# Performance work log

Measured on AMD Instinct MI355X. Metric: run time of the kernel, lower is better.

The kernel has to match this reference:

```python
import jax, jax.numpy as jnp
import numpy as np

E, K, H, I = 16, 4, 2048, 1024
B, S = 1, 2048


def setup_inputs() -> dict:
    key = jax.random.key(0)
    ks = jax.random.split(key, 5)
    scale_in = 1.0 / np.sqrt(H)
    scale_mid = 1.0 / np.sqrt(I)
    return {
        "x": jax.random.normal(ks[0], (B, S, H), dtype=jnp.float32),
        "gate_w": jax.random.normal(ks[1], (E, H), dtype=jnp.float32) * scale_in,
        "w1_gate": jax.random.normal(ks[2], (E, I, H), dtype=jnp.float32) * scale_in,
        "w1_up": jax.random.normal(ks[3], (E, I, H), dtype=jnp.float32) * scale_in,
        "w2": jax.random.normal(ks[4], (E, H, I), dtype=jnp.float32) * scale_mid,
        "topk": K,
    }


def reference(x, gate_w, w1_gate, w1_up, w2, topk):
    orig_shape = x.shape
    xt = x.reshape(-1, x.shape[-1])            # [T, H]
    T = xt.shape[0]
    n_exp = gate_w.shape[0]

    # Router: top-k logits, softmax over the selected k (as in the torch code).
    logits = xt @ gate_w.T                      # [T, E]
    topk_vals, topk_ids = jax.lax.top_k(logits, topk)
    topk_w = jax.nn.softmax(topk_vals, axis=-1)  # [T, K]

    # Dense per-token-per-expert combine weight; 0 for unselected experts.
    # Mathematically identical to the gather/scatter-add loop: unselected
    # experts contribute expert_out * 0.
    gate_dense = jnp.zeros((T, n_exp), dtype=xt.dtype)
    gate_dense = gate_dense.at[jnp.arange(T)[:, None], topk_ids].add(topk_w)

    # SwiGLU per expert (dense over experts; weights zero-out unused ones).
    g = jnp.einsum("th,eih->tei", xt, w1_gate)   # [T, E, I]
    u = jnp.einsum("th,eih->tei", xt, w1_up)     # [T, E, I]
    h = jax.nn.silu(g) * u                        # [T, E, I]
    out = jnp.einsum("tei,te,ehi->th", h, gate_dense, w2)  # [T, H]
    return out.reshape(orig_shape)
```

## Files before the change

kernel.cpp:

```cpp
#include <hip/hip_runtime.h>
#include <hip/hip_bf16.h>
#include <stdint.h>

#define NEXP 16
#define KSEL 4
#define HDIM 2048
#define IDIM 1024
#define TTOK 2048
#define NT1 16
#define NTB 16
#define MAXT1 47
#define MAXB1 (MAXT1 * NT1)
#define MAXBB (MAXT1 * NTB)
#define NCVT 1024
#define NCVT1 512
#define NW8 ((NEXP * IDIM * HDIM) / 8)

typedef __attribute__((ext_vector_type(8))) short bf16x8;
typedef __attribute__((ext_vector_type(4))) float f32x4;
typedef unsigned int u32;

__device__ __forceinline__ uint32_t pack2(float a, float b) {
  __hip_bfloat162 h = __float22bfloat162_rn(float2{a, b});
  uint32_t u;
  __builtin_memcpy(&u, &h, 4);
  return u;
}
__device__ __forceinline__ ushort bf1(float a) {
  __hip_bfloat16 h = __float2bfloat16(a);
  ushort u;
  __builtin_memcpy(&u, &h, 2);
  return u;
}
__device__ __forceinline__ void gload16(const void* g, void* l) {
  __builtin_amdgcn_global_load_lds(
      (const __attribute__((address_space(1))) u32*)g,
      (__attribute__((address_space(3))) u32*)l, 16, 0, 0);
}
__device__ __forceinline__ int swzread(int row, int q) {
  return row * 32 + ((q ^ ((row >> 1) & 3)) << 3);
}
__device__ __forceinline__ void cvt_bodyN(const float* __restrict__ src,
                                          ushort* __restrict__ dst,
                                          int idx0, int stride) {
  for (int i = idx0; i < NW8; i += stride) {
    f32x4 a = __builtin_nontemporal_load(((const f32x4*)src) + i * 2);
    f32x4 b = __builtin_nontemporal_load(((const f32x4*)src) + i * 2 + 1);
    uint4 t;
    t.x = pack2(a[0], a[1]); t.y = pack2(a[2], a[3]);
    t.z = pack2(b[0], b[1]); t.w = pack2(b[2], b[3]);
    ((uint4*)dst)[i] = t;
  }
}

__global__ __launch_bounds__(256) void router_kernel(
    const float* __restrict__ x, const float* __restrict__ gw,
    ushort* __restrict__ xb, int* __restrict__ topk_id,
    float* __restrict__ topk_w,
    const float* __restrict__ srcG, ushort* __restrict__ dstG,
    const float* __restrict__ srcU, ushort* __restrict__ dstU)
{
  if (blockIdx.x >= TTOK / 4 + NCVT) {
    cvt_bodyN(srcU, dstU,
              (blockIdx.x - (TTOK / 4 + NCVT)) * 256 + threadIdx.x, NCVT * 256);
    return;
  }
  if (blockIdx.x >= TTOK / 4) {
    cvt_bodyN(srcG, dstG,
              (blockIdx.x - TTOK / 4) * 256 + threadIdx.x, NCVT * 256);
    return;
  }
  const int wid = threadIdx.x >> 6;
  const int lane = threadIdx.x & 63;
  const int t = blockIdx.x * 4 + wid;
  const float4* x4 = (const float4*)(x + (size_t)t * HDIM);
  const float4* gw4 = (const float4*)gw;
  float acc[NEXP];
#pragma unroll
  for (int e = 0; e < NEXP; ++e) acc[e] = 0.f;
#pragma unroll
  for (int i = 0; i < HDIM / 256; ++i) {
    const int idx = i * 64 + lane;
    float4 xv = x4[idx];
    uint2 xp;
    xp.x = pack2(xv.x, xv.y);
    xp.y = pack2(xv.z, xv.w);
    *(uint2*)(xb + (size_t)t * HDIM + idx * 4) = xp;
#pragma unroll
    for (int e = 0; e < NEXP; ++e) {
      float4 wv = gw4[e * (HDIM / 4) + idx];
      acc[e] += xv.x * wv.x + xv.y * wv.y + xv.z * wv.z + xv.w * wv.w;
    }
  }
#pragma unroll
  for (int e = 0; e < NEXP; ++e) {
#pragma unroll
    for (int off = 32; off >= 1; off >>= 1)
      acc[e] += __shfl_xor(acc[e], off);
  }
  if (lane == 0) {
    unsigned taken = 0;
    float vals[KSEL];
    int ids[KSEL];
#pragma unroll
    for (int k = 0; k < KSEL; ++k) {
      float bv = -3.4e38f; int bi = 0;
      for (int e = 0; e < NEXP; ++e)
        if (!((taken >> e) & 1u) && acc[e] > bv) { bv = acc[e]; bi = e; }
      taken |= 1u << bi; vals[k] = bv; ids[k] = bi;
    }
    float m = vals[0], s = 0.f, w[KSEL];
#pragma unroll
    for (int k = 0; k < KSEL; ++k) { w[k] = __expf(vals[k] - m); s += w[k]; }
    float is = 1.f / s;
#pragma unroll
    for (int k = 0; k < KSEL; ++k) {
      topk_id[t * KSEL + k] = ids[k];
      topk_w[t * KSEL + k] = w[k] * is;
    }
  }
}

__global__ __launch_bounds__(1024) void plan_scatter_kernel(
    const int* __restrict__ topk_id, int* __restrict__ counts,
    int* __restrict__ offsets, int* __restrict__ nWA, int* __restrict__ nWB,
    int* __restrict__ wlA, int* __restrict__ wlB,
    int* __restrict__ rowTok, int* __restrict__ inv)
{
  __shared__ int cnt[NEXP], off[NEXP], cur[NEXP];
  __shared__ int t1[NEXP], p1[NEXP];
  const int tid = threadIdx.x;
  if (tid < NEXP) { cnt[tid] = 0; cur[tid] = 0; }
  __syncthreads();
  for (int i = tid; i < TTOK * KSEL; i += 1024)
    atomicAdd(&cnt[topk_id[i]], 1);
  __syncthreads();
  if (tid == 0) {
    int s = 0, a = 0;
    for (int e = 0; e < NEXP; ++e) {
      off[e] = s; s += cnt[e];
      t1[e] = (cnt[e] + 255) >> 8;  p1[e] = a;  a += t1[e];
    }
    *nWA = a * NT1;
    *nWB = a * NTB;
  }
  __syncthreads();
  if (tid < NEXP) {
    counts[tid] = cnt[tid];
    offsets[tid] = off[tid];
    const int e = tid, T = t1[e];
    int idx = p1[e] * NT1;
    for (int nt = 0; nt < NT1; ++nt)
      for (int mt = 0; mt < T; ++mt)
        wlA[idx++] = (e << 12) | (nt << 6) | mt;
  } else if (tid < 2 * NEXP) {
    const int e = tid - NEXP, T = t1[e];
    int idx = p1[e] * NTB;
    for (int nt = 0; nt < NTB; ++nt)
      for (int mt = 0; mt < T; ++mt)
        wlB[idx++] = (e << 12) | (nt << 6) | mt;
  }
  for (int i = tid; i < TTOK * KSEL; i += 1024) {
    const int e = topk_id[i];
    const int pos = atomicAdd(&cur[e], 1);
    const int row = off[e] + pos;
    rowTok[row] = i >> 2;
    inv[i] = row;
  }
}

__global__ __launch_bounds__(512) void gemm1_kernel(
    const ushort* __restrict__ xb,
    const ushort* __restrict__ wG, const ushort* __restrict__ wU,
    const int* __restrict__ rowTok, const int* __restrict__ counts,
    const int* __restrict__ offsets, const int* __restrict__ nW,
    const int* __restrict__ wl, ushort* __restrict__ hbuf,
    const float* __restrict__ cvsrc, ushort* __restrict__ cvdst)
{
  if (blockIdx.x >= MAXB1) {
    cvt_bodyN(cvsrc, cvdst,
              (blockIdx.x - MAXB1) * 512 + threadIdx.x, NCVT1 * 512);
    return;
  }
  const int nTot = *nW;
  const int L = (blockIdx.x & 7) * (MAXB1 / 8) + (blockIdx.x >> 3);
  if (L >= nTot) return;
  const int w = wl[L];
  const int e = w >> 12, nt = (w >> 6) & 63, mt = w & 63;
  const int n_e = counts[e], rowbase = offsets[e];

  __shared__ ushort As[2][256 * 32];
  __shared__ ushort Bg[2][64 * 32];
  __shared__ ushort Bu[2][64 * 32];

  const int tid = threadIdx.x;
  const int lane = tid & 63;
  const int wid = tid >> 6;

  const int lr4 = lane >> 2;
  const int ckA = lane & 3;
  const int arl0 = wid * 32 + lr4;
  const int arl1 = wid * 32 + 16 + lr4;
  const int schA0 = (ckA ^ ((arl0 >> 1) & 3)) << 3;
  const int schA1 = (ckA ^ ((arl1 >> 1) & 3)) << 3;
  const int ag0 = mt * 256 + arl0, ag1 = mt * 256 + arl1;
  const int tok0 = rowTok[rowbase + (ag0 < n_e ? ag0 : n_e - 1)];
  const int tok1 = rowTok[rowbase + (ag1 < n_e ? ag1 : n_e - 1)];
  const ushort* pA0 = xb + (size_t)tok0 * HDIM + schA0;
  const ushort* pA1 = xb + (size_t)tok1 * HDIM + schA1;
  const int brl = (wid & 3) * 16 + lr4;
  const int schB = (ckA ^ ((brl >> 1) & 3)) << 3;
  const size_t wbase = (size_t)e * IDIM * HDIM;
  const ushort* pB = ((wid < 4) ? wG : wU) + wbase +
                     (size_t)(nt * 64 + brl) * HDIM + schB;

  const int wr = (wid >> 1) << 6;
  const int wc = (wid & 1) << 5;
  const int lr = lane & 15;
  const int q = lane >> 4;

  f32x4 accG[4][2], accU[4][2];
#pragma unroll
  for (int i = 0; i < 4; ++i)
#pragma unroll
    for (int j = 0; j < 2; ++j) {
      accG[i][j] = (f32x4){0.f, 0.f, 0.f, 0.f};
      accU[i][j] = (f32x4){0.f, 0.f, 0.f, 0.f};
    }

  auto STAGE = [&](int b) {
    gload16(pA0, &As[b][wid * 1024 + lane * 8]);
    gload16(pA1, &As[b][wid * 1024 + 512 + lane * 8]);
    if (wid < 4) gload16(pB, &Bg[b][wid * 512 + lane * 8]);
    else         gload16(pB, &Bu[b][(wid - 4) * 512 + lane * 8]);
    pA0 += 32; pA1 += 32; pB += 32;
  };

  const int NTK = HDIM / 32;
  STAGE(0);
  __syncthreads();
  int buf = 0;
  for (int kt = 0; kt < NTK; ++kt) {
    if (kt + 1 < NTK) STAGE(buf ^ 1);
    bf16x8 af[4], bg[2], bu[2];
#pragma unroll
    for (int mi = 0; mi < 4; ++mi)
      af[mi] = *(const bf16x8*)&As[buf][swzread(wr + mi * 16 + lr, q)];
#pragma unroll
    for (int ni = 0; ni < 2; ++ni) {
      bg[ni] = *(const bf16x8*)&Bg[buf][swzread(wc + ni * 16 + lr, q)];
      bu[ni] = *(const bf16x8*)&Bu[buf][swzread(wc + ni * 16 + lr, q)];
    }
#pragma unroll
    for (int mi = 0; mi < 4; ++mi)
#pragma unroll
      for (int ni = 0; ni < 2; ++ni) {
        accG[mi][ni] = __builtin_amdgcn_mfma_f32_16x16x32_bf16(af[mi], bg[ni], accG[mi][ni], 0, 0, 0);
        accU[mi][ni] = __builtin_amdgcn_mfma_f32_16x16x32_bf16(af[mi], bu[ni], accU[mi][ni], 0, 0, 0);
      }
    __syncthreads();
    buf ^= 1;
  }

#pragma unroll
  for (int mi = 0; mi < 4; ++mi) {
#pragma unroll
    for (int ni = 0; ni < 2; ++ni) {
      const int col = nt * 64 + wc + ni * 16 + lr;
#pragma unroll
      for (int r = 0; r < 4; ++r) {
        const int mrow = mt * 256 + wr + mi * 16 + q * 4 + r;
        if (mrow < n_e) {
          const float gv = accG[mi][ni][r];
          const float uv = accU[mi][ni][r];
          const float hv = (gv / (1.f + __expf(-gv))) * uv;
          hbuf[(size_t)(rowbase + mrow) * IDIM + col] = bf1(hv);
        }
      }
    }
  }
}

__global__ __launch_bounds__(512) void gemmB_kernel(
    const ushort* __restrict__ hb, const ushort* __restrict__ wb,
    const int* __restrict__ counts, const int* __restrict__ offsets,
    const int* __restrict__ nW, const int* __restrict__ wl,
    ushort* __restrict__ po)
{
  const int nTot = *nW;
  const int L = (blockIdx.x & 7) * (MAXBB / 8) + (blockIdx.x >> 3);
  if (L >= nTot) return;
  const int w = wl[L];
  const int e = w >> 12, nt = (w >> 6) & 63, mt = w & 63;
  const int n_e = counts[e], rowbase = offsets[e];

  __shared__ ushort As[2][256 * 32];
  __shared__ ushort Bs[2][128 * 32];

  const int tid = threadIdx.x;
  const int lane = tid & 63;
  const int wid = tid >> 6;

  const int lr4 = lane >> 2;
  const int ckA = lane & 3;
  const int arl0 = wid * 32 + lr4;
  const int arl1 = wid * 32 + 16 + lr4;
  const int schA0 = (ckA ^ ((arl0 >> 1) & 3)) << 3;
  const int schA1 = (ckA ^ ((arl1 >> 1) & 3)) << 3;
  const int ag0 = mt * 256 + arl0, ag1 = mt * 256 + arl1;
  const int g0 = rowbase + (ag0 < n_e ? ag0 : n_e - 1);
  const int g1 = rowbase + (ag1 < n_e ? ag1 : n_e - 1);
  const ushort* pA0 = hb + (size_t)g0 * IDIM + schA0;
  const ushort* pA1 = hb + (size_t)g1 * IDIM + schA1;
  const int brl = wid * 16 + lr4;
  const int schB = (ckA ^ ((brl >> 1) & 3)) << 3;
  const size_t wbase = (size_t)e * HDIM * IDIM;
  const ushort* pB = wb + wbase + (size_t)(nt * 128 + brl) * IDIM + schB;

  const int wr = (wid >> 1) << 6;
  const int wc = (wid & 1) << 6;
  const int lr = lane & 15;
  const int q = lane >> 4;

  f32x4 acc[4][4];
#pragma unroll
  for (int i = 0; i < 4; ++i)
#pragma unroll
    for (int j = 0; j < 4; ++j) acc[i][j] = (f32x4){0.f, 0.f, 0.f, 0.f};

  auto STAGE = [&](int b) {
    gload16(pA0, &As[b][wid * 1024 + lane * 8]);
    gload16(pA1, &As[b][wid * 1024 + 512 + lane * 8]);
    gload16(pB, &Bs[b][wid * 512 + lane * 8]);
    pA0 += 32; pA1 += 32; pB += 32;
  };

  const int NTK = IDIM / 32;
  STAGE(0);
  __syncthreads();
  int buf = 0;
  for (int kt = 0; kt < NTK; ++kt) {
    if (kt + 1 < NTK) STAGE(buf ^ 1);
    bf16x8 af[4], bfr[4];
#pragma unroll
    for (int mi = 0; mi < 4; ++mi)
      af[mi] = *(const bf16x8*)&As[buf][swzread(wr + mi * 16 + lr, q)];
#pragma unroll
    for (int ni = 0; ni < 4; ++ni)
      bfr[ni] = *(const bf16x8*)&Bs[buf][swzread(wc + ni * 16 + lr, q)];
#pragma unroll
    for (int mi = 0; mi < 4; ++mi)
#pragma unroll
      for (int ni = 0; ni < 4; ++ni)
        acc[mi][ni] = __builtin_amdgcn_mfma_f32_16x16x32_bf16(af[mi], bfr[ni], acc[mi][ni], 0, 0, 0);
    __syncthreads();
    buf ^= 1;
  }

#pragma unroll
  for (int mi = 0; mi < 4; ++mi) {
#pragma unroll
    for (int ni = 0; ni < 4; ++ni) {
      const int col = nt * 128 + wc + ni * 16 + lr;
#pragma unroll
      for (int r = 0; r < 4; ++r) {
        const int mrow = mt * 256 + wr + mi * 16 + q * 4 + r;
        if (mrow < n_e)
          po[(size_t)(rowbase + mrow) * HDIM + col] = bf1(acc[mi][ni][r]);
      }
    }
  }
}

__global__ __launch_bounds__(256) void combine_kernel(
    const ushort* __restrict__ po, const int* __restrict__ inv,
    const float* __restrict__ tw, float* __restrict__ out)
{
  const int t = blockIdx.x;
  const int r0 = inv[t * 4 + 0], r1 = inv[t * 4 + 1];
  const int r2 = inv[t * 4 + 2], r3 = inv[t * 4 + 3];
  const float w0 = tw[t * 4 + 0], w1 = tw[t * 4 + 1];
  const float w2v = tw[t * 4 + 2], w3 = tw[t * 4 + 3];
  const int i = threadIdx.x;
  uint4 v0 = *(const uint4*)(po + (size_t)r0 * HDIM + i * 8);
  uint4 v1 = *(const uint4*)(po + (size_t)r1 * HDIM + i * 8);
  uint4 v2 = *(const uint4*)(po + (size_t)r2 * HDIM + i * 8);
  uint4 v3 = *(const uint4*)(po + (size_t)r3 * HDIM + i * 8);
  float o[8];
#pragma unroll
  for (int w = 0; w < 4; ++w) {
    const uint32_t a = (&v0.x)[w], b = (&v1.x)[w], c = (&v2.x)[w], d = (&v3.x)[w];
    o[w * 2 + 0] = w0 * __builtin_bit_cast(float, a << 16) +
                   w1 * __builtin_bit_cast(float, b << 16) +
                   w2v * __builtin_bit_cast(float, c << 16) +
                   w3 * __builtin_bit_cast(float, d << 16);
    o[w * 2 + 1] = w0 * __builtin_bit_cast(float, a & 0xffff0000u) +
                   w1 * __builtin_bit_cast(float, b & 0xffff0000u) +
                   w2v * __builtin_bit_cast(float, c & 0xffff0000u) +
                   w3 * __builtin_bit_cast(float, d & 0xffff0000u);
  }
  float4* o4 = (float4*)(out + (size_t)t * HDIM + i * 8);
  o4[0] = (float4){o[0], o[1], o[2], o[3]};
  o4[1] = (float4){o[4], o[5], o[6], o[7]};
}

extern "C" void kernel_launch(void* const* d_in, const int* in_sizes, int n_in,
                              void* d_out, int out_size, void* d_ws, size_t ws_size,
                              hipStream_t stream) {
  const float* x   = (const float*)d_in[0];
  const float* gw  = (const float*)d_in[1];
  const float* w1g = (const float*)d_in[2];
  const float* w1u = (const float*)d_in[3];
  const float* w2  = (const float*)d_in[4];
  float* out = (float*)d_out;

  char* ws = (char*)d_ws;
  ushort* xb    = (ushort*)(ws + 0);
  ushort* wbufG = (ushort*)(ws + 8388608);
  ushort* wbufU = (ushort*)(ws + 75497472);
  ushort* wbuf2 = (ushort*)(ws + 142606336);
  ushort* hbuf  = (ushort*)(ws + 209715200);
  ushort* po    = (ushort*)(ws + 226492416);
  int*    tkid   = (int*)(ws + 260046848);
  float*  tkw    = (float*)(ws + 260046848 + 32768);
  int*    rowTok = (int*)(ws + 260046848 + 65536);
  int*    inv    = (int*)(ws + 260046848 + 98304);
  int*    ctrl   = (int*)(ws + 260177920);
  int* counts  = ctrl;
  int* offsets = ctrl + 32;
  int* nWA     = ctrl + 50;
  int* nWB     = ctrl + 51;
  int* wlA     = ctrl + 64;
  int* wlB     = ctrl + 64 + MAXB1;

  router_kernel<<<TTOK / 4 + 2 * NCVT, 256, 0, stream>>>(
      x, gw, xb, tkid, tkw, w1g, wbufG, w1u, wbufU);
  plan_scatter_kernel<<<1, 1024, 0, stream>>>(tkid, counts, offsets, nWA, nWB,
                                              wlA, wlB, rowTok, inv);
  gemm1_kernel<<<MAXB1 + NCVT1, 512, 0, stream>>>(
      xb, wbufG, wbufU, rowTok, counts, offsets, nWA, wlA, hbuf,
      w2, wbuf2);
  gemmB_kernel<<<MAXBB, 512, 0, stream>>>(hbuf, wbuf2, counts, offsets,
                                          nWB, wlB, po);
  combine_kernel<<<TTOK, 256, 0, stream>>>(po, inv, tkw, out);
}
```

Baseline: 310.2 us.

## Restructure gemm1 into 128-row tiles with triple-buffered loads and split gate/up waves

The first MoE GEMM drops from 256-row to 128-row M tiles, which roughly doubles its grid and gives it a separate worklist size from the second GEMM. Its shared-memory pipeline goes from double to triple buffering, with explicit vmcnt waits and raw barriers so two stages of loads stay in flight. Each wave now computes either the gate or the up product instead of both, and the up results are passed through LDS to the gate waves for the SwiGLU epilogue. This aims at more parallelism and better latency hiding, at the cost of an extra LDS exchange plus barrier and lower arithmetic reuse per tile.

After: 309.4 us. Within noise of the previous version (-0.2%).

```diff
diff --git a/kernel.cpp b/kernel.cpp
--- a/kernel.cpp
+++ b/kernel.cpp
@@ -9,9 +9,10 @@
 #define TTOK 2048
 #define NT1 16
 #define NTB 16
-#define MAXT1 47
+#define MAXT1 80
 #define MAXB1 (MAXT1 * NT1)
-#define MAXBB (MAXT1 * NTB)
+#define MAXTB 47
+#define MAXBB (MAXTB * NTB)
 #define NCVT 1024
 #define NCVT1 512
 #define NW8 ((NEXP * IDIM * HDIM) / 8)
@@ -128,7 +129,7 @@
     int* __restrict__ rowTok, int* __restrict__ inv)
 {
   __shared__ int cnt[NEXP], off[NEXP], cur[NEXP];
-  __shared__ int t1[NEXP], p1[NEXP];
+  __shared__ int t1[NEXP], p1[NEXP], tB[NEXP], pB[NEXP];
   const int tid = threadIdx.x;
   if (tid < NEXP) { cnt[tid] = 0; cur[tid] = 0; }
   __syncthreads();
@@ -136,13 +137,14 @@
     atomicAdd(&cnt[topk_id[i]], 1);
   __syncthreads();
   if (tid == 0) {
-    int s = 0, a = 0;
+    int s = 0, a = 0, b = 0;
     for (int e = 0; e < NEXP; ++e) {
       off[e] = s; s += cnt[e];
-      t1[e] = (cnt[e] + 255) >> 8;  p1[e] = a;  a += t1[e];
+      t1[e] = (cnt[e] + 127) >> 7;  p1[e] = a;  a += t1[e];
+      tB[e] = (cnt[e] + 255) >> 8;  pB[e] = b;  b += tB[e];
     }
     *nWA = a * NT1;
-    *nWB = a * NTB;
+    *nWB = b * NTB;
   }
   __syncthreads();
   if (tid < NEXP) {
@@ -154,8 +156,8 @@
       for (int mt = 0; mt < T; ++mt)
         wlA[idx++] = (e << 12) | (nt << 6) | mt;
   } else if (tid < 2 * NEXP) {
-    const int e = tid - NEXP, T = t1[e];
-    int idx = p1[e] * NTB;
+    const int e = tid - NEXP, T = tB[e];
+    int idx = pB[e] * NTB;
     for (int nt = 0; nt < NTB; ++nt)
       for (int mt = 0; mt < T; ++mt)
         wlB[idx++] = (e << 12) | (nt << 6) | mt;
@@ -189,96 +191,119 @@
   const int e = w >> 12, nt = (w >> 6) & 63, mt = w & 63;
   const int n_e = counts[e], rowbase = offsets[e];
 
-  __shared__ ushort As[2][256 * 32];
-  __shared__ ushort Bg[2][64 * 32];
-  __shared__ ushort Bu[2][64 * 32];
+  __shared__ ushort lds[24576];
+#define AS(b) (lds + (b) * 4096)
+#define BG(b) (lds + 12288 + (b) * 2048)
+#define BU(b) (lds + 18432 + (b) * 2048)
 
   const int tid = threadIdx.x;
   const int lane = tid & 63;
-  const int wid = tid >> 6;
-
-  const int lr4 = lane >> 2;
-  const int ckA = lane & 3;
-  const int arl0 = wid * 32 + lr4;
-  const int arl1 = wid * 32 + 16 + lr4;
-  const int schA0 = (ckA ^ ((arl0 >> 1) & 3)) << 3;
-  const int schA1 = (ckA ^ ((arl1 >> 1) & 3)) << 3;
-  const int ag0 = mt * 256 + arl0, ag1 = mt * 256 + arl1;
-  const int tok0 = rowTok[rowbase + (ag0 < n_e ? ag0 : n_e - 1)];
-  const int tok1 = rowTok[rowbase + (ag1 < n_e ? ag1 : n_e - 1)];
-  const ushort* pA0 = xb + (size_t)tok0 * HDIM + schA0;
-  const ushort* pA1 = xb + (size_t)tok1 * HDIM + schA1;
-  const int brl = (wid & 3) * 16 + lr4;
-  const int schB = (ckA ^ ((brl >> 1) & 3)) << 3;
+  const int wv = tid >> 6;
+
+  const int arow = tid >> 2;
+  const int ckA = tid & 3;
+  const int schA = (ckA ^ ((arow >> 1) & 3)) << 3;
+  const int agr = mt * 128 + arow;
+  const int tokA = rowTok[rowbase + (agr < n_e ? agr : n_e - 1)];
+  const ushort* pA = xb + (size_t)tokA * HDIM + schA;
+  const int bloc = tid & 255;
+  const int brow = bloc >> 2;
+  const int ckB = bloc & 3;
+  const int schB = (ckB ^ ((brow >> 1) & 3)) << 3;
   const size_t wbase = (size_t)e * IDIM * HDIM;
-  const ushort* pB = ((wid < 4) ? wG : wU) + wbase +
-                     (size_t)(nt * 64 + brl) * HDIM + schB;
-
-  const int wr = (wid >> 1) << 6;
-  const int wc = (wid & 1) << 5;
+  const ushort* pB = ((tid < 256) ? wG : wU) + wbase +
+                     (size_t)(nt * 64 + brow) * HDIM + schB;
+
+  const int wr = (wv >> 2) << 6;
+  const int ng = wv & 3;
+  const bool isU = ng >= 2;
+  const int wc = (ng & 1) << 5;
   const int lr = lane & 15;
   const int q = lane >> 4;
 
-  f32x4 accG[4][2], accU[4][2];
+  f32x4 acc[4][2];
 #pragma unroll
   for (int i = 0; i < 4; ++i)
 #pragma unroll
-    for (int j = 0; j < 2; ++j) {
-      accG[i][j] = (f32x4){0.f, 0.f, 0.f, 0.f};
-      accU[i][j] = (f32x4){0.f, 0.f, 0.f, 0.f};
-    }
+    for (int j = 0; j < 2; ++j) acc[i][j] = (f32x4){0.f, 0.f, 0.f, 0.f};
 
   auto STAGE = [&](int b) {
-    gload16(pA0, &As[b][wid * 1024 + lane * 8]);
-    gload16(pA1, &As[b][wid * 1024 + 512 + lane * 8]);
-    if (wid < 4) gload16(pB, &Bg[b][wid * 512 + lane * 8]);
-    else         gload16(pB, &Bu[b][(wid - 4) * 512 + lane * 8]);
-    pA0 += 32; pA1 += 32; pB += 32;
+    gload16(pA, AS(b) + tid * 8);
+    if (tid < 256) gload16(pB, BG(b) + bloc * 8);
+    else           gload16(pB, BU(b) + bloc * 8);
+    pA += 32; pB += 32;
   };
 
   const int NTK = HDIM / 32;
   STAGE(0);
-  __syncthreads();
+  STAGE(1);
+  asm volatile("s_waitcnt vmcnt(2)" ::: "memory");
+  __builtin_amdgcn_s_barrier();
+  __builtin_amdgcn_sched_barrier(0);
   int buf = 0;
   for (int kt = 0; kt < NTK; ++kt) {
-    if (kt + 1 < NTK) STAGE(buf ^ 1);
-    bf16x8 af[4], bg[2], bu[2];
-#pragma unroll
-    for (int mi = 0; mi < 4; ++mi)
-      af[mi] = *(const bf16x8*)&As[buf][swzread(wr + mi * 16 + lr, q)];
-#pragma unroll
-    for (int ni = 0; ni < 2; ++ni) {
-      bg[ni] = *(const bf16x8*)&Bg[buf][swzread(wc + ni * 16 + lr, q)];
-      bu[ni] = *(const bf16x8*)&Bu[buf][swzread(wc + ni * 16 + lr, q)];
-    }
+    if (kt + 2 < NTK) STAGE(buf == 0 ? 2 : buf - 1);
+    const ushort* bsrc = isU ? BU(buf) : BG(buf);
+    bf16x8 af[4], bf[2];
+#pragma unroll
+    for (int mi = 0; mi < 4; ++mi)
+      af[mi] = *(const bf16x8*)&AS(buf)[swzread(wr + mi * 16 + lr, q)];
+#pragma unroll
+    for (int ni = 0; ni < 2; ++ni)
+      bf[ni] = *(const bf16x8*)&bsrc[swzread(wc + ni * 16 + lr, q)];
+#pragma unroll
+    for (int mi = 0; mi < 4; ++mi)
+#pragma unroll
+      for (int ni = 0; ni < 2; ++ni)
+        acc[mi][ni] = __builtin_amdgcn_mfma_f32_16x16x32_bf16(af[mi], bf[ni], acc[mi][ni], 0, 0, 0);
+    if (kt + 1 < NTK) {
+      if (kt + 2 < NTK)
+        asm volatile("s_waitcnt vmcnt(2)" ::: "memory");
+      else
+        asm volatile("s_waitcnt vmcnt(0)" ::: "memory");
+      __builtin_amdgcn_s_barrier();
+      __builtin_amdgcn_sched_barrier(0);
+    }
+    buf = (buf == 2) ? 0 : buf + 1;
+  }
+
+  __syncthreads();
+  float* uex = (float*)lds;
+  if (isU) {
+    const int ucol0 = ((ng - 2) << 5);
+#pragma unroll
+    for (int mi = 0; mi < 4; ++mi)
+#pragma unroll
+      for (int ni = 0; ni < 2; ++ni)
+#pragma unroll
+        for (int r = 0; r < 4; ++r)
+          uex[(wr + mi * 16 + q * 4 + r) * 64 + ucol0 + ni * 16 + lr] = acc[mi][ni][r];
+  }
+  __syncthreads();
+  if (!isU) {
+    const int gcol0 = (ng << 5);
 #pragma unroll
     for (int mi = 0; mi < 4; ++mi)
 #pragma unroll
       for (int ni = 0; ni < 2; ++ni) {
-        accG[mi][ni] = __builtin_amdgcn_mfma_f32_16x16x32_bf16(af[mi], bg[ni], accG[mi][ni], 0, 0, 0);
-        accU[mi][ni] = __builtin_amdgcn_mfma_f32_16x16x32_bf16(af[mi], bu[ni], accU[mi][ni], 0, 0, 0);
-      }
-    __syncthreads();
-    buf ^= 1;
-  }
-
-#pragma unroll
-  for (int mi = 0; mi < 4; ++mi) {
-#pragma unroll
-    for (int ni = 0; ni < 2; ++ni) {
-      const int col = nt * 64 + wc + ni * 16 + lr;
-#pragma unroll
-      for (int r = 0; r < 4; ++r) {
-        const int mrow = mt * 256 + wr + mi * 16 + q * 4 + r;
-        if (mrow < n_e) {
-          const float gv = accG[mi][ni][r];
-          const float uv = accU[mi][ni][r];
-          const float hv = (gv / (1.f + __expf(-gv))) * uv;
-          hbuf[(size_t)(rowbase + mrow) * IDIM + col] = bf1(hv);
+        const int lcol = gcol0 + ni * 16 + lr;
+        const int col = nt * 64 + lcol;
+#pragma unroll
+        for (int r = 0; r < 4; ++r) {
+          const int lrow = wr + mi * 16 + q * 4 + r;
+          const int mrow = mt * 128 + lrow;
+          if (mrow < n_e) {
+            const float gv = acc[mi][ni][r];
+            const float uv = uex[lrow * 64 + lcol];
+            const float hv = (gv / (1.f + __expf(-gv))) * uv;
+            hbuf[(size_t)(rowbase + mrow) * IDIM + col] = bf1(hv);
+          }
         }
       }
-    }
-  }
+  }
+#undef AS
+#undef BG
+#undef BU
 }
 
 __global__ __launch_bounds__(512) void gemmB_kernel(
```
